# Kernel tuning notes

Measured on AMD Instinct MI355X. Metric: run time of the kernel, lower is better.

Reference implementation:

```python
import math
import jax, jax.numpy as jnp
import numpy as np

B, L, D, H = 2, 2048, 512, 8
HD = D // H
PADDING_IDX = 0


def _sinusoid_table(num_embeddings, dim, padding_idx):
    # matches RelativeSinusoidalPositionalEmbedding.get_embedding
    half = dim // 2
    inv = math.log(10000.0) / (half - 1)
    freqs = jnp.exp(jnp.arange(half, dtype=jnp.float32) * (-inv))
    ang = jnp.arange(num_embeddings, dtype=jnp.float32)[:, None] * freqs[None, :]
    emb = jnp.concatenate([jnp.sin(ang), jnp.cos(ang)], axis=1)  # [N, dim]
    return emb.at[padding_idx].set(0.0)


def _rel_pos_embed(seq_len):
    # RelativeEmbedding.forward: init table size 513 (origin_shift=257); since
    # padding_idx + seq_len > 257 it regenerates with num_embeddings = 2*seq_len,
    # origin_shift = seq_len. All static at trace time.
    init_origin = 512 // 2 + 1
    if PADDING_IDX + seq_len > init_origin:
        num = (PADDING_IDX + seq_len) * 2
        origin = num // 2
    else:
        num = 512 + 1
        origin = init_origin
    table = _sinusoid_table(num, HD, PADDING_IDX)
    positions = jnp.arange(-seq_len, seq_len) + origin  # [2L]
    return table[positions]  # [2L, HD]


def _shift(BD):
    # [B,H,L,2L] -> [B,H,L,L], Transformer-XL relative shift
    b, h, l, _ = BD.shape
    BD = jnp.concatenate([BD, jnp.zeros((b, h, l, 1), BD.dtype)], axis=-1)
    BD = BD.reshape(b, h, -1, l)[:, :, :-1].reshape(b, h, l, -1)
    return BD[:, :, :, l:]


def setup_inputs() -> dict:
    key = jax.random.key(0)
    ks = jax.random.split(key, 7)
    s = 1.0 / math.sqrt(D)
    return {
        "q": jax.random.normal(ks[0], (B, L, D), jnp.float32),
        "k": jax.random.normal(ks[1], (B, L, D), jnp.float32),
        "mask": jnp.ones((B, L, L), jnp.int32),
        "Wq": jax.random.normal(ks[2], (D, D), jnp.float32) * s,
        "Wkv": jax.random.normal(ks[3], (2 * D, D), jnp.float32) * s,
        "Wr": jax.random.normal(ks[4], (HD, HD), jnp.float32) * (1.0 / math.sqrt(HD)),
        "r_r_bias": jax.random.normal(ks[5], (H, HD), jnp.float32) * 0.1,
        "r_w_bias": jax.random.normal(ks[6], (H, HD), jnp.float32) * 0.1,
    }


def reference(q, k, mask, Wq, Wkv, Wr, r_r_bias, r_w_bias):
    b, l, d = q.shape
    scale = math.sqrt(HD)

    pos = _rel_pos_embed(l)                # [2L, HD]
    r = pos @ Wr.T                          # [2L, HD]

    qp = q @ Wq.T                           # [B,L,D]
    kv = k @ Wkv.T                          # [B,L,2D]
    kk, vv = jnp.split(kv, 2, axis=-1)

    qh = qp.reshape(b, l, H, HD).transpose(0, 2, 1, 3)  # [B,H,L,HD]
    kh = kk.reshape(b, l, H, HD).transpose(0, 2, 1, 3)
    vh = vv.reshape(b, l, H, HD).transpose(0, 2, 1, 3)

    rw_head_q = qh + r_r_bias[None, :, None, :]
    AC = jnp.einsum('bnqd,bnkd->bnqk', rw_head_q, kh)        # [B,H,L,L]
    D_ = jnp.einsum('nd,ld->nl', r_w_bias, r)[None, :, None, :]  # [1,H,1,2L]
    B_ = jnp.einsum('bnqd,ld->bnql', qh, r)                  # [B,H,L,2L]
    BD = _shift(B_ + D_)                                      # [B,H,L,L]

    attn = (AC + BD) / scale
    attn = jnp.where(mask[:, None, :, :] == 0, -jnp.inf, attn)
    attn = jax.nn.softmax(attn, axis=-1)

    out = jnp.einsum('bnqk,bnkd->bnqd', attn, vh)
    out = out.transpose(0, 2, 1, 3).reshape(b, l, d)
    return (out, attn)
```

## Files before the change

kernel.cpp:

```cpp
#include <hip/hip_runtime.h>
#include <math.h>

#define NL 2048
#define N2L 4096

typedef __attribute__((ext_vector_type(8))) short bf16x8;
typedef __attribute__((ext_vector_type(4))) float f32x4;
#define MFMA(a,b,c) __builtin_amdgcn_mfma_f32_16x16x32_bf16((a),(b),(c),0,0,0)

#define BARRIER() do {                                        \
    __builtin_amdgcn_sched_barrier(0);                        \
    asm volatile("s_waitcnt lgkmcnt(0)" ::: "memory");        \
    __builtin_amdgcn_s_barrier();                             \
    __builtin_amdgcn_sched_barrier(0);                        \
  } while (0)

__device__ __forceinline__ unsigned short bf16_rne(float x){
  unsigned int u = __float_as_uint(x);
  u += 0x7FFFu + ((u>>16)&1u);
  return (unsigned short)(u>>16);
}
__device__ __forceinline__ float bf16_to_f(unsigned short h){
  return __uint_as_float(((unsigned int)h)<<16);
}

__global__ __launch_bounds__(256) void split_kernel(
    const float* __restrict__ q, const float* __restrict__ k,
    const float* __restrict__ Wq, const float* __restrict__ Wkv,
    unsigned short* __restrict__ qsh, unsigned short* __restrict__ qsl,
    unsigned short* __restrict__ ksh, unsigned short* __restrict__ ksl,
    unsigned short* __restrict__ wqh, unsigned short* __restrict__ wql,
    unsigned short* __restrict__ wkh, unsigned short* __restrict__ wkl) {
  const int C1 = 524288, C2 = 1048576, C3 = 1114112, C4 = 1245184;
  for (int i = blockIdx.x * blockDim.x + threadIdx.x; i < C4; i += gridDim.x * blockDim.x) {
    const float* src; unsigned short *dh, *dl; int j;
    if (i < C1)      { src = q;   dh = qsh; dl = qsl; j = i; }
    else if (i < C2) { src = k;   dh = ksh; dl = ksl; j = i - C1; }
    else if (i < C3) { src = Wq;  dh = wqh; dl = wql; j = i - C2; }
    else             { src = Wkv; dh = wkh; dl = wkl; j = i - C3; }
    float4 v = reinterpret_cast<const float4*>(src)[j];
    unsigned short h0 = bf16_rne(v.x), h1 = bf16_rne(v.y), h2 = bf16_rne(v.z), h3 = bf16_rne(v.w);
    unsigned short l0 = bf16_rne(v.x - bf16_to_f(h0));
    unsigned short l1 = bf16_rne(v.y - bf16_to_f(h1));
    unsigned short l2 = bf16_rne(v.z - bf16_to_f(h2));
    unsigned short l3 = bf16_rne(v.w - bf16_to_f(h3));
    reinterpret_cast<uint2*>(dh)[j] = make_uint2((unsigned)h0 | ((unsigned)h1 << 16),
                                                 (unsigned)h2 | ((unsigned)h3 << 16));
    reinterpret_cast<uint2*>(dl)[j] = make_uint2((unsigned)l0 | ((unsigned)l1 << 16),
                                                 (unsigned)l2 | ((unsigned)l3 << 16));
  }
}

__global__ void build_r_kernel(const float* __restrict__ Wr,
                               unsigned short* __restrict__ rh,
                               unsigned short* __restrict__ rl) {
  int n = blockIdx.x;
  int t = threadIdx.x;
  __shared__ float pos[64];
  float v = 0.f;
  if (n != 0) {
    int j = t & 31;
    float inv = logf(10000.f) * (1.0f / 31.0f);
    float freq = expf(-inv * (float)j);
    float ang = (float)n * freq;
    v = (t < 32) ? sinf(ang) : cosf(ang);
  }
  pos[t] = v;
  __syncthreads();
  float acc = 0.f;
  const float* wrow = Wr + t * 64;
  #pragma unroll
  for (int j = 0; j < 64; ++j) acc += pos[j] * wrow[j];
  unsigned short hh = bf16_rne(acc);
  rh[n * 64 + t] = hh;
  rl[n * 64 + t] = bf16_rne(acc - bf16_to_f(hh));
}

__global__ __launch_bounds__(256) void proj_kernel(
    const unsigned short* __restrict__ qsh, const unsigned short* __restrict__ qsl,
    const unsigned short* __restrict__ ksh, const unsigned short* __restrict__ ksl,
    const unsigned short* __restrict__ wqh, const unsigned short* __restrict__ wql,
    const unsigned short* __restrict__ wkh, const unsigned short* __restrict__ wkl,
    const float* __restrict__ rrb, const float* __restrict__ rwb,
    unsigned short* __restrict__ qAh, unsigned short* __restrict__ qAl,
    unsigned short* __restrict__ qBh, unsigned short* __restrict__ qBl,
    unsigned short* __restrict__ khh, unsigned short* __restrict__ khl,
    unsigned short* __restrict__ vTh, unsigned short* __restrict__ vTl) {
  int tid = threadIdx.x;
  int w = tid >> 6, lane = tid & 63, li = lane & 15, g = lane >> 4;
  int bx = blockIdx.x, by = blockIdx.y;
  f32x4 acc[4];
  #pragma unroll
  for (int i = 0; i < 4; ++i) { acc[i][0]=0.f; acc[i][1]=0.f; acc[i][2]=0.f; acc[i][3]=0.f; }

  if (by < 16) {
    int n0 = by * 64, m0 = bx * 64;
    const unsigned short* Xh = (n0 < 512) ? qsh : ksh;
    const unsigned short* Xl = (n0 < 512) ? qsl : ksl;
    const unsigned short* Wh = (n0 < 512) ? (wqh + (size_t)n0 * 512) : (wkh + (size_t)(n0 - 512) * 512);
    const unsigned short* Wl = (n0 < 512) ? (wql + (size_t)n0 * 512) : (wkl + (size_t)(n0 - 512) * 512);
    int rowm = m0 + 16 * w + li;
    for (int ks = 0; ks < 16; ++ks) {
      int d0 = ks * 32 + 8 * g;
      bf16x8 ah = *(const bf16x8*)(Xh + (size_t)rowm * 512 + d0);
      bf16x8 al = *(const bf16x8*)(Xl + (size_t)rowm * 512 + d0);
      #pragma unroll
      for (int nt = 0; nt < 4; ++nt) {
        bf16x8 bh_ = *(const bf16x8*)(Wh + (size_t)(16 * nt + li) * 512 + d0);
        bf16x8 bl_ = *(const bf16x8*)(Wl + (size_t)(16 * nt + li) * 512 + d0);
        acc[nt] = MFMA(ah, bh_, acc[nt]);
        acc[nt] = MFMA(al, bh_, acc[nt]);
        acc[nt] = MFMA(ah, bl_, acc[nt]);
      }
    }
    if (n0 < 512) {
      int h = n0 >> 6;
      #pragma unroll
      for (int nt = 0; nt < 4; ++nt) {
        int d = 16 * nt + li;
        float rrv = rrb[h * 64 + d], rwv = rwb[h * 64 + d];
        #pragma unroll
        for (int r = 0; r < 4; ++r) {
          int m = m0 + 16 * w + 4 * g + r;
          int b = m >> 11, lt = m & 2047;
          size_t base = (((size_t)(b * 8 + h)) * 2048 + lt) * 64 + d;
          float a1 = acc[nt][r] + rrv;
          unsigned short h1 = bf16_rne(a1);
          qAh[base] = h1; qAl[base] = bf16_rne(a1 - bf16_to_f(h1));
          float a2 = acc[nt][r] + rwv;
          unsigned short h2 = bf16_rne(a2);
          qBh[base] = h2; qBl[base] = bf16_rne(a2 - bf16_to_f(h2));
        }
      }
    } else {
      int h = (n0 - 512) >> 6;
      #pragma unroll
      for (int nt = 0; nt < 4; ++nt) {
        int d = 16 * nt + li;
        #pragma unroll
        for (int r = 0; r < 4; ++r) {
          int m = m0 + 16 * w + 4 * g + r;
          int b = m >> 11, lt = m & 2047;
          size_t base = (((size_t)(b * 8 + h)) * 2048 + lt) * 64 + d;
          unsigned short h1 = bf16_rne(acc[nt][r]);
          khh[base] = h1; khl[base] = bf16_rne(acc[nt][r] - bf16_to_f(h1));
        }
      }
    }
  } else {
    int fy = by - 16, m0 = bx * 64, f0 = fy * 64;
    const unsigned short* Ah = wkh + (size_t)(512 + f0 + 16 * w + li) * 512;
    const unsigned short* Al = wkl + (size_t)(512 + f0 + 16 * w + li) * 512;
    for (int ks = 0; ks < 16; ++ks) {
      int d0 = ks * 32 + 8 * g;
      bf16x8 ah = *(const bf16x8*)(Ah + d0);
      bf16x8 al = *(const bf16x8*)(Al + d0);
      #pragma unroll
      for (int nt = 0; nt < 4; ++nt) {
        bf16x8 bh_ = *(const bf16x8*)(ksh + (size_t)(m0 + 16 * nt + li) * 512 + d0);
        bf16x8 bl_ = *(const bf16x8*)(ksl + (size_t)(m0 + 16 * nt + li) * 512 + d0);
        acc[nt] = MFMA(ah, bh_, acc[nt]);
        acc[nt] = MFMA(al, bh_, acc[nt]);
        acc[nt] = MFMA(ah, bl_, acc[nt]);
      }
    }
    int h = fy;
    #pragma unroll
    for (int nt = 0; nt < 4; ++nt) {
      int m = m0 + 16 * nt + li;
      int b = m >> 11, lt = m & 2047;
      #pragma unroll
      for (int r = 0; r < 4; ++r) {
        int d = 16 * w + 4 * g + r;
        size_t base = (((size_t)(b * 8 + h)) * 64 + d) * 2048 + lt;
        unsigned short h1 = bf16_rne(acc[nt][r]);
        vTh[base] = h1; vTl[base] = bf16_rne(acc[nt][r] - bf16_to_f(h1));
      }
    }
  }
}

__global__ __launch_bounds__(256) void attn_kernel(
    const unsigned short* __restrict__ qAh, const unsigned short* __restrict__ qAl,
    const unsigned short* __restrict__ qBh, const unsigned short* __restrict__ qBl,
    const unsigned short* __restrict__ khh, const unsigned short* __restrict__ khl,
    const unsigned short* __restrict__ vTh, const unsigned short* __restrict__ vTl,
    const unsigned short* __restrict__ rh, const unsigned short* __restrict__ rl,
    const int* __restrict__ mask, float* __restrict__ attnp,
    float* __restrict__ oPart, float* __restrict__ rlbuf) {
  __shared__ float TPbuf[3264];
  __shared__ float Slds[2048];

  float* Tlds = TPbuf;

  int tid = threadIdx.x;
  int w = tid >> 6, lane = tid & 63, li = lane & 15, g = lane >> 4;
  int qlc = tid >> 3, jc = tid & 7, kc = jc * 8;
  int q0 = blockIdx.x * 32;
  int y = blockIdx.y, kh = y & 1, bh = y >> 1, b = bh >> 3;
  const unsigned short* qAhp = qAh + (size_t)bh * 131072;
  const unsigned short* qAlp = qAl + (size_t)bh * 131072;
  const unsigned short* qBhp = qBh + (size_t)bh * 131072;
  const unsigned short* qBlp = qBl + (size_t)bh * 131072;
  const unsigned short* khhp = khh + (size_t)bh * 131072;
  const unsigned short* khlp = khl + (size_t)bh * 131072;
  const unsigned short* vThp = vTh + (size_t)bh * 131072;
  const unsigned short* vTlp = vTl + (size_t)bh * 131072;
  const int* mrow = mask + (size_t)b * NL * NL + (size_t)(q0 + qlc) * NL;
  float* arow = attnp + (size_t)bh * NL * NL + (size_t)(q0 + qlc) * NL;

  bf16x8 fAh[2][2], fAl[2][2], fBh[2][2], fBl[2][2];
  #pragma unroll
  for (int nt = 0; nt < 2; ++nt)
    #pragma unroll
    for (int ks = 0; ks < 2; ++ks) {
      size_t o = (size_t)(q0 + 16 * nt + li) * 64 + 32 * ks + 8 * g;
      fAh[nt][ks] = *(const bf16x8*)(qAhp + o);
      fAl[nt][ks] = *(const bf16x8*)(qAlp + o);
      fBh[nt][ks] = *(const bf16x8*)(qBhp + o);
      fBl[nt][ks] = *(const bf16x8*)(qBlp + o);
    }

  unsigned int sread0 = (unsigned)(qlc * 256 + (((2 * jc) * 16) ^ ((qlc & 7) << 4)));
  unsigned int sread1 = (unsigned)(qlc * 256 + (((2 * jc + 1) * 16) ^ ((qlc & 7) << 4)));
  unsigned int woff = (unsigned)(qlc * 128 + ((kc * 2) ^ ((qlc & 7) << 4)));

  float lrun = 0.f;
  f32x4 accO[2];
  #pragma unroll
  for (int i = 0; i < 2; ++i) { accO[i][0]=0.f; accO[i][1]=0.f; accO[i][2]=0.f; accO[i][3]=0.f; }

  int kt0 = kh * 16;
  for (int kt = kt0; kt < kt0 + 16; ++kt) {
    int k0 = kt * 64;
    int4 mv1 = *(const int4*)(mrow + k0 + kc);
    int4 mv2 = *(const int4*)(mrow + k0 + kc + 4);
    bf16x8 vhf[2], vlf[2];
    #pragma unroll
    for (int ks = 0; ks < 2; ++ks) {
      size_t vo = (size_t)(16 * w + li) * NL + k0 + 32 * ks + 8 * g;
      vhf[ks] = *(const bf16x8*)(vThp + vo);
      vlf[ks] = *(const bf16x8*)(vTlp + vo);
    }
    int krow = k0 + 16 * w + li;
    f32x4 accS[2];
    #pragma unroll
    for (int i = 0; i < 2; ++i) { accS[i][0]=0.f; accS[i][1]=0.f; accS[i][2]=0.f; accS[i][3]=0.f; }
    __builtin_amdgcn_s_setprio(1);
    #pragma unroll
    for (int ks = 0; ks < 2; ++ks) {
      size_t o = (size_t)krow * 64 + 32 * ks + 8 * g;
      bf16x8 ah = *(const bf16x8*)(khhp + o);
      bf16x8 al = *(const bf16x8*)(khlp + o);
      #pragma unroll
      for (int nt = 0; nt < 2; ++nt) {
        accS[nt] = MFMA(ah, fAh[nt][ks], accS[nt]);
        accS[nt] = MFMA(al, fAh[nt][ks], accS[nt]);
        accS[nt] = MFMA(ah, fAl[nt][ks], accS[nt]);
      }
    }
    int nlo = k0 - q0 + 2016;
    f32x4 accT[3];
    #pragma unroll
    for (int i = 0; i < 3; ++i) { accT[i][0]=0.f; accT[i][1]=0.f; accT[i][2]=0.f; accT[i][3]=0.f; }
    #pragma unroll
    for (int pp = 0; pp < 3; ++pp) {
      int pi = w * 3 + pp, jt = pi >> 1, ntp = pi & 1;
      int rrow = nlo + jt * 16 + li;
      #pragma unroll
      for (int ks = 0; ks < 2; ++ks) {
        size_t o = (size_t)rrow * 64 + 32 * ks + 8 * g;
        bf16x8 ah = *(const bf16x8*)(rh + o);
        bf16x8 al = *(const bf16x8*)(rl + o);
        accT[pp] = MFMA(ah, fBh[ntp][ks], accT[pp]);
        accT[pp] = MFMA(al, fBh[ntp][ks], accT[pp]);
        accT[pp] = MFMA(ah, fBl[ntp][ks], accT[pp]);
      }
    }
    __builtin_amdgcn_s_setprio(0);
    #pragma unroll
    for (int pp = 0; pp < 3; ++pp) {
      int pi = w * 3 + pp, jt = pi >> 1, ntp = pi & 1;
      #pragma unroll
      for (int r = 0; r < 4; ++r)
        Tlds[(jt * 16 + 4 * g + r) * 34 + ntp * 16 + li] = accT[pp][r];
    }
    BARRIER();
    #pragma unroll
    for (int nt = 0; nt < 2; ++nt) {
      int ql_ = 16 * nt + li;
      float sv[4];
      #pragma unroll
      for (int r = 0; r < 4; ++r) {
        int kl = 16 * w + 4 * g + r;
        sv[r] = (accS[nt][r] + Tlds[(kl - ql_ + 32) * 34 + ql_]) * 0.125f;
      }
      unsigned int so = (unsigned)(ql_ * 256 + (((4 * w + g) * 16) ^ ((ql_ & 7) << 4)));
      *(float4*)((char*)Slds + so) = make_float4(sv[0], sv[1], sv[2], sv[3]);
    }
    BARRIER();
    float4 sa = *(const float4*)((const char*)Slds + sread0);
    float4 sb = *(const float4*)((const char*)Slds + sread1);
    float p0 = mv1.x ? __expf(sa.x) : 0.f;
    float p1 = mv1.y ? __expf(sa.y) : 0.f;
    float p2 = mv1.z ? __expf(sa.z) : 0.f;
    float p3 = mv1.w ? __expf(sa.w) : 0.f;
    float p4 = mv2.x ? __expf(sb.x) : 0.f;
    float p5 = mv2.y ? __expf(sb.y) : 0.f;
    float p6 = mv2.z ? __expf(sb.z) : 0.f;
    float p7 = mv2.w ? __expf(sb.w) : 0.f;
    *(float4*)(arow + k0 + kc) = make_float4(p0, p1, p2, p3);
    *(float4*)(arow + k0 + kc + 4) = make_float4(p4, p5, p6, p7);
    float ts = p0 + p1 + p2 + p3 + p4 + p5 + p6 + p7;
    ts += __shfl_xor(ts, 1);
    ts += __shfl_xor(ts, 2);
    ts += __shfl_xor(ts, 4);
    lrun += ts;
    unsigned short h0 = bf16_rne(p0), h1 = bf16_rne(p1), h2 = bf16_rne(p2), h3 = bf16_rne(p3);
    unsigned short h4 = bf16_rne(p4), h5 = bf16_rne(p5), h6 = bf16_rne(p6), h7 = bf16_rne(p7);
    unsigned short e0 = bf16_rne(p0 - bf16_to_f(h0)), e1 = bf16_rne(p1 - bf16_to_f(h1));
    unsigned short e2 = bf16_rne(p2 - bf16_to_f(h2)), e3 = bf16_rne(p3 - bf16_to_f(h3));
    unsigned short e4 = bf16_rne(p4 - bf16_to_f(h4)), e5 = bf16_rne(p5 - bf16_to_f(h5));
    unsigned short e6 = bf16_rne(p6 - bf16_to_f(h6)), e7 = bf16_rne(p7 - bf16_to_f(h7));
    *(uint4*)((char*)TPbuf + woff) =
        make_uint4((unsigned)h0 | ((unsigned)h1 << 16), (unsigned)h2 | ((unsigned)h3 << 16),
                   (unsigned)h4 | ((unsigned)h5 << 16), (unsigned)h6 | ((unsigned)h7 << 16));
    *(uint4*)((char*)TPbuf + 4096 + woff) =
        make_uint4((unsigned)e0 | ((unsigned)e1 << 16), (unsigned)e2 | ((unsigned)e3 << 16),
                   (unsigned)e4 | ((unsigned)e5 << 16), (unsigned)e6 | ((unsigned)e7 << 16));
    BARRIER();
    __builtin_amdgcn_s_setprio(1);
    #pragma unroll
    for (int ks = 0; ks < 2; ++ks) {
      #pragma unroll
      for (int nt = 0; nt < 2; ++nt) {
        unsigned int ro = (unsigned)((16 * nt + li) * 128 + (((32 * ks + 8 * g) * 2) ^ ((li & 7) << 4)));
        bf16x8 ph = *(const bf16x8*)((const char*)TPbuf + ro);
        bf16x8 pl = *(const bf16x8*)((const char*)TPbuf + 4096 + ro);
        accO[nt] = MFMA(vhf[ks], ph, accO[nt]);
        accO[nt] = MFMA(vlf[ks], ph, accO[nt]);
        accO[nt] = MFMA(vhf[ks], pl, accO[nt]);
      }
    }
    __builtin_amdgcn_s_setprio(0);
    BARRIER();
  }

  if (jc == 0)
    rlbuf[(size_t)kh * 32768 + (size_t)bh * 2048 + q0 + qlc] = lrun;
  float* op = oPart + (size_t)kh * 2097152 + (size_t)bh * 131072;
  #pragma unroll
  for (int nt = 0; nt < 2; ++nt) {
    int qg = q0 + 16 * nt + li;
    int d = 16 * w + 4 * g;
    *(float4*)(op + (size_t)qg * 64 + d) =
        make_float4(accO[nt][0], accO[nt][1], accO[nt][2], accO[nt][3]);
  }
}

__global__ __launch_bounds__(256) void combine_kernel(
    const float* __restrict__ oPart, const float* __restrict__ rlbuf,
    float* __restrict__ outp) {
  int bh = blockIdx.y, b = bh >> 3, h = bh & 7;
  int q = blockIdx.x * 4 + (threadIdx.x >> 6);
  int d = threadIdx.x & 63;
  size_t i0 = ((size_t)bh * 2048 + q) * 64 + d;
  float l = rlbuf[(size_t)bh * 2048 + q] + rlbuf[32768 + (size_t)bh * 2048 + q];
  float o = oPart[i0] + oPart[2097152 + i0];
  outp[((size_t)b * 2048 + q) * 512 + h * 64 + d] = o / l;
}

__global__ __launch_bounds__(256) void rescale_kernel(
    const float* __restrict__ rlbuf, float* __restrict__ attnp) {
  int row = blockIdx.x;
  int bh = blockIdx.y;
  float rv = 1.0f / (rlbuf[(size_t)bh * 2048 + row] + rlbuf[32768 + (size_t)bh * 2048 + row]);
  float* ap = attnp + ((size_t)bh * NL + row) * NL + threadIdx.x * 8;
  float4 a = *(float4*)ap;
  float4 b2 = *(float4*)(ap + 4);
  *(float4*)ap = make_float4(a.x * rv, a.y * rv, a.z * rv, a.w * rv);
  *(float4*)(ap + 4) = make_float4(b2.x * rv, b2.y * rv, b2.z * rv, b2.w * rv);
}

extern "C" void kernel_launch(void* const* d_in, const int* in_sizes, int n_in,
                              void* d_out, int out_size, void* d_ws, size_t ws_size,
                              hipStream_t stream) {
  const float* q    = (const float*)d_in[0];
  const float* k    = (const float*)d_in[1];
  const int*   mask = (const int*)d_in[2];
  const float* Wq   = (const float*)d_in[3];
  const float* Wkv  = (const float*)d_in[4];
  const float* Wr   = (const float*)d_in[5];
  const float* rrb  = (const float*)d_in[6];
  const float* rwb  = (const float*)d_in[7];

  float* outp  = (float*)d_out;
  float* attnp = outp + (size_t)2 * NL * 512;

  unsigned short* W = (unsigned short*)d_ws;
  const size_t RHI = 0,            RLO = RHI + 262144;
  const size_t QSH = RLO + 262144, QSL = QSH + 2097152;
  const size_t KSH = QSL + 2097152, KSL = KSH + 2097152;
  const size_t WQH = KSL + 2097152, WQL = WQH + 262144;
  const size_t WKH = WQL + 262144,  WKL = WKH + 524288;
  const size_t QAH = WKL + 524288,  QAL = QAH + 2097152;
  const size_t QBH = QAL + 2097152, QBL = QBH + 2097152;
  const size_t KHH = QBL + 2097152, KHL = KHH + 2097152;
  const size_t VTH = KHL + 2097152, VTL = VTH + 2097152;
  const size_t RLB = VTL + 2097152;
  float* rlbuf = (float*)(W + RLB);
  float* oPart = (float*)(W + QSH);

  hipLaunchKernelGGL(split_kernel, dim3(1024), dim3(256), 0, stream,
                     q, k, Wq, Wkv, W+QSH, W+QSL, W+KSH, W+KSL, W+WQH, W+WQL, W+WKH, W+WKL);
  hipLaunchKernelGGL(build_r_kernel, dim3(N2L), dim3(64), 0, stream, Wr, W+RHI, W+RLO);
  hipLaunchKernelGGL(proj_kernel, dim3(64, 24), dim3(256), 0, stream,
                     W+QSH, W+QSL, W+KSH, W+KSL, W+WQH, W+WQL, W+WKH, W+WKL, rrb, rwb,
                     W+QAH, W+QAL, W+QBH, W+QBL, W+KHH, W+KHL, W+VTH, W+VTL);
  hipLaunchKernelGGL(attn_kernel, dim3(64, 32), dim3(256), 0, stream,
                     W+QAH, W+QAL, W+QBH, W+QBL, W+KHH, W+KHL, W+VTH, W+VTL,
                     W+RHI, W+RLO, mask, attnp, oPart, rlbuf);
  hipLaunchKernelGGL(combine_kernel, dim3(512, 16), dim3(256), 0, stream,
                     oPart, rlbuf, outp);
  hipLaunchKernelGGL(rescale_kernel, dim3(NL, 16), dim3(256), 0, stream,
                     rlbuf, attnp);
}
```

Baseline: 596.2 us.

## Fold positional bias into per-head table and reuse the Q fragment for both score terms

```diff
diff --git a/kernel.cpp b/kernel.cpp
--- a/kernel.cpp
+++ b/kernel.cpp
@@ -52,8 +52,11 @@
 }
 
 __global__ void build_r_kernel(const float* __restrict__ Wr,
+                               const float* __restrict__ rrb,
+                               const float* __restrict__ rwb,
                                unsigned short* __restrict__ rh,
-                               unsigned short* __restrict__ rl) {
+                               unsigned short* __restrict__ rl,
+                               float* __restrict__ cTab) {
   int n = blockIdx.x;
   int t = threadIdx.x;
   __shared__ float pos[64];
@@ -74,6 +77,13 @@
   unsigned short hh = bf16_rne(acc);
   rh[n * 64 + t] = hh;
   rl[n * 64 + t] = bf16_rne(acc - bf16_to_f(hh));
+  #pragma unroll
+  for (int h = 0; h < 8; ++h) {
+    float pr = acc * (rwb[h * 64 + t] - rrb[h * 64 + t]);
+    #pragma unroll
+    for (int off = 1; off < 64; off <<= 1) pr += __shfl_xor(pr, off);
+    if (t == 0) cTab[h * N2L + n] = pr;
+  }
 }
 
 __global__ __launch_bounds__(256) void proj_kernel(
@@ -81,9 +91,8 @@
     const unsigned short* __restrict__ ksh, const unsigned short* __restrict__ ksl,
     const unsigned short* __restrict__ wqh, const unsigned short* __restrict__ wql,
     const unsigned short* __restrict__ wkh, const unsigned short* __restrict__ wkl,
-    const float* __restrict__ rrb, const float* __restrict__ rwb,
+    const float* __restrict__ rrb,
     unsigned short* __restrict__ qAh, unsigned short* __restrict__ qAl,
-    unsigned short* __restrict__ qBh, unsigned short* __restrict__ qBl,
     unsigned short* __restrict__ khh, unsigned short* __restrict__ khl,
     unsigned short* __restrict__ vTh, unsigned short* __restrict__ vTl) {
   int tid = threadIdx.x;
@@ -118,7 +127,7 @@
       #pragma unroll
       for (int nt = 0; nt < 4; ++nt) {
         int d = 16 * nt + li;
-        float rrv = rrb[h * 64 + d], rwv = rwb[h * 64 + d];
+        float rrv = rrb[h * 64 + d];
         #pragma unroll
         for (int r = 0; r < 4; ++r) {
           int m = m0 + 16 * w + 4 * g + r;
@@ -127,9 +136,6 @@
           float a1 = acc[nt][r] + rrv;
           unsigned short h1 = bf16_rne(a1);
           qAh[base] = h1; qAl[base] = bf16_rne(a1 - bf16_to_f(h1));
-          float a2 = acc[nt][r] + rwv;
-          unsigned short h2 = bf16_rne(a2);
-          qBh[base] = h2; qBl[base] = bf16_rne(a2 - bf16_to_f(h2));
         }
       }
     } else {
@@ -180,14 +186,13 @@
   }
 }
 
-__global__ __launch_bounds__(256) void attn_kernel(
+__global__ __launch_bounds__(256, 4) void attn_kernel(
     const unsigned short* __restrict__ qAh, const unsigned short* __restrict__ qAl,
-    const unsigned short* __restrict__ qBh, const unsigned short* __restrict__ qBl,
     const unsigned short* __restrict__ khh, const unsigned short* __restrict__ khl,
     const unsigned short* __restrict__ vTh, const unsigned short* __restrict__ vTl,
     const unsigned short* __restrict__ rh, const unsigned short* __restrict__ rl,
-    const int* __restrict__ mask, float* __restrict__ attnp,
-    float* __restrict__ oPart, float* __restrict__ rlbuf) {
+    const float* __restrict__ cTab, const int* __restrict__ mask,
+    float* __restrict__ attnp, float* __restrict__ oPart, float* __restrict__ rlbuf) {
   __shared__ float TPbuf[3264];
   __shared__ float Slds[2048];
 
@@ -197,19 +202,18 @@
   int w = tid >> 6, lane = tid & 63, li = lane & 15, g = lane >> 4;
   int qlc = tid >> 3, jc = tid & 7, kc = jc * 8;
   int q0 = blockIdx.x * 32;
-  int y = blockIdx.y, kh = y & 1, bh = y >> 1, b = bh >> 3;
+  int y = blockIdx.y, kh = y & 1, bh = y >> 1, b = bh >> 3, h = bh & 7;
   const unsigned short* qAhp = qAh + (size_t)bh * 131072;
   const unsigned short* qAlp = qAl + (size_t)bh * 131072;
-  const unsigned short* qBhp = qBh + (size_t)bh * 131072;
-  const unsigned short* qBlp = qBl + (size_t)bh * 131072;
   const unsigned short* khhp = khh + (size_t)bh * 131072;
   const unsigned short* khlp = khl + (size_t)bh * 131072;
   const unsigned short* vThp = vTh + (size_t)bh * 131072;
   const unsigned short* vTlp = vTl + (size_t)bh * 131072;
+  const float* cTabh = cTab + (size_t)h * N2L;
   const int* mrow = mask + (size_t)b * NL * NL + (size_t)(q0 + qlc) * NL;
   float* arow = attnp + (size_t)bh * NL * NL + (size_t)(q0 + qlc) * NL;
 
-  bf16x8 fAh[2][2], fAl[2][2], fBh[2][2], fBl[2][2];
+  bf16x8 fAh[2][2], fAl[2][2];
   #pragma unroll
   for (int nt = 0; nt < 2; ++nt)
     #pragma unroll
@@ -217,8 +221,6 @@
       size_t o = (size_t)(q0 + 16 * nt + li) * 64 + 32 * ks + 8 * g;
       fAh[nt][ks] = *(const bf16x8*)(qAhp + o);
       fAl[nt][ks] = *(const bf16x8*)(qAlp + o);
-      fBh[nt][ks] = *(const bf16x8*)(qBhp + o);
-      fBl[nt][ks] = *(const bf16x8*)(qBlp + o);
     }
 
   unsigned int sread0 = (unsigned)(qlc * 256 + (((2 * jc) * 16) ^ ((qlc & 7) << 4)));
@@ -233,6 +235,7 @@
   int kt0 = kh * 16;
   for (int kt = kt0; kt < kt0 + 16; ++kt) {
     int k0 = kt * 64;
+    int nlo = k0 - q0 + 2016;
     int4 mv1 = *(const int4*)(mrow + k0 + kc);
     int4 mv2 = *(const int4*)(mrow + k0 + kc + 4);
     bf16x8 vhf[2], vlf[2];
@@ -242,6 +245,12 @@
       vhf[ks] = *(const bf16x8*)(vThp + vo);
       vlf[ks] = *(const bf16x8*)(vTlp + vo);
     }
+    float4 cvs[3];
+    #pragma unroll
+    for (int pp = 0; pp < 3; ++pp) {
+      int pi = w * 3 + pp, jt = pi >> 1;
+      cvs[pp] = *(const float4*)(cTabh + nlo + jt * 16 + 4 * g);
+    }
     int krow = k0 + 16 * w + li;
     f32x4 accS[2];
     #pragma unroll
@@ -259,7 +268,6 @@
         accS[nt] = MFMA(ah, fAl[nt][ks], accS[nt]);
       }
     }
-    int nlo = k0 - q0 + 2016;
     f32x4 accT[3];
     #pragma unroll
     for (int i = 0; i < 3; ++i) { accT[i][0]=0.f; accT[i][1]=0.f; accT[i][2]=0.f; accT[i][3]=0.f; }
@@ -272,18 +280,19 @@
         size_t o = (size_t)rrow * 64 + 32 * ks + 8 * g;
         bf16x8 ah = *(const bf16x8*)(rh + o);
         bf16x8 al = *(const bf16x8*)(rl + o);
-        accT[pp] = MFMA(ah, fBh[ntp][ks], accT[pp]);
-        accT[pp] = MFMA(al, fBh[ntp][ks], accT[pp]);
-        accT[pp] = MFMA(ah, fBl[ntp][ks], accT[pp]);
+        accT[pp] = MFMA(ah, fAh[ntp][ks], accT[pp]);
+        accT[pp] = MFMA(al, fAh[ntp][ks], accT[pp]);
+        accT[pp] = MFMA(ah, fAl[ntp][ks], accT[pp]);
       }
     }
     __builtin_amdgcn_s_setprio(0);
     #pragma unroll
     for (int pp = 0; pp < 3; ++pp) {
       int pi = w * 3 + pp, jt = pi >> 1, ntp = pi & 1;
+      const float* cv = (const float*)&cvs[pp];
       #pragma unroll
       for (int r = 0; r < 4; ++r)
-        Tlds[(jt * 16 + 4 * g + r) * 34 + ntp * 16 + li] = accT[pp][r];
+        Tlds[(jt * 16 + 4 * g + r) * 34 + ntp * 16 + li] = accT[pp][r] + cv[r];
     }
     BARRIER();
     #pragma unroll
@@ -404,22 +413,24 @@
   const size_t WQH = KSL + 2097152, WQL = WQH + 262144;
   const size_t WKH = WQL + 262144,  WKL = WKH + 524288;
   const size_t QAH = WKL + 524288,  QAL = QAH + 2097152;
-  const size_t QBH = QAL + 2097152, QBL = QBH + 2097152;
-  const size_t KHH = QBL + 2097152, KHL = KHH + 2097152;
+  const size_t KHH = QAL + 2097152, KHL = KHH + 2097152;
   const size_t VTH = KHL + 2097152, VTL = VTH + 2097152;
   const size_t RLB = VTL + 2097152;
+  const size_t CTB = RLB + 131072;
   float* rlbuf = (float*)(W + RLB);
+  float* cTab  = (float*)(W + CTB);
   float* oPart = (float*)(W + QSH);
 
   hipLaunchKernelGGL(split_kernel, dim3(1024), dim3(256), 0, stream,
                      q, k, Wq, Wkv, W+QSH, W+QSL, W+KSH, W+KSL, W+WQH, W+WQL, W+WKH, W+WKL);
-  hipLaunchKernelGGL(build_r_kernel, dim3(N2L), dim3(64), 0, stream, Wr, W+RHI, W+RLO);
+  hipLaunchKernelGGL(build_r_kernel, dim3(N2L), dim3(64), 0, stream,
+                     Wr, rrb, rwb, W+RHI, W+RLO, cTab);
   hipLaunchKernelGGL(proj_kernel, dim3(64, 24), dim3(256), 0, stream,
-                     W+QSH, W+QSL, W+KSH, W+KSL, W+WQH, W+WQL, W+WKH, W+WKL, rrb, rwb,
-                     W+QAH, W+QAL, W+QBH, W+QBL, W+KHH, W+KHL, W+VTH, W+VTL);
+                     W+QSH, W+QSL, W+KSH, W+KSL, W+WQH, W+WQL, W+WKH, W+WKL, rrb,
+                     W+QAH, W+QAL, W+KHH, W+KHL, W+VTH, W+VTL);
   hipLaunchKernelGGL(attn_kernel, dim3(64, 32), dim3(256), 0, stream,
-                     W+QAH, W+QAL, W+QBH, W+QBL, W+KHH, W+KHL, W+VTH, W+VTL,
-                     W+RHI, W+RLO, mask, attnp, oPart, rlbuf);
+                     W+QAH, W+QAL, W+KHH, W+KHL, W+VTH, W+VTL,
+                     W+RHI, W+RLO, cTab, mask, attnp, oPart, rlbuf);
   hipLaunchKernelGGL(combine_kernel, dim3(512, 16), dim3(256), 0, stream,
                      oPart, rlbuf, outp);
   hipLaunchKernelGGL(rescale_kernel, dim3(NL, 16), dim3(256), 0, stream,
```

Result: slower. 866.8 us (+45.4%).
